# Performance work log

Measured on AMD Instinct MI355X. Metric: run time of the kernel, lower is better.

The kernel has to match this reference:

```python
import jax, jax.numpy as jnp
import numpy as np

N_NODES = 50000
N_EDGES = 800000
DIM = 128
NUM_GRAPHS = 512


def setup_inputs() -> dict:
    key = jax.random.key(0)
    ks = jax.random.split(key, 12)
    s = 1.0 / np.sqrt(DIM)
    inp = {
        'x': jax.random.normal(ks[0], (N_NODES, DIM), dtype=jnp.float32),
        'edge_index': jax.random.randint(ks[1], (2, N_EDGES), 0, N_NODES, dtype=jnp.int32),
        'batch': jnp.sort(jax.random.randint(ks[2], (N_NODES,), 0, NUM_GRAPHS, dtype=jnp.int32)),
        'W1a': jax.random.uniform(ks[3], (DIM, DIM), jnp.float32, -s, s),
        'b1a': jax.random.uniform(ks[4], (DIM,), jnp.float32, -s, s),
        'W1b': jax.random.uniform(ks[5], (DIM, DIM), jnp.float32, -s, s),
        'b1b': jax.random.uniform(ks[6], (DIM,), jnp.float32, -s, s),
        'W2a': jax.random.uniform(ks[7], (DIM, DIM), jnp.float32, -s, s),
        'b2a': jax.random.uniform(ks[8], (DIM,), jnp.float32, -s, s),
        'W2b': jax.random.uniform(ks[9], (DIM, DIM), jnp.float32, -s, s),
        'b2b': jax.random.uniform(ks[10], (DIM,), jnp.float32, -s, s),
    }
    return inp


def _gin_conv(x, edge_index, Wa, ba, Wb, bb):
    # GINConv with eps=0: h_i = MLP(x_i + sum_{j->i} x_j)
    src, dst = edge_index[0], edge_index[1]
    agg = jax.ops.segment_sum(x[src], dst, num_segments=x.shape[0])  # [N, F]
    h = x + agg
    h = jax.nn.relu(h @ Wa + ba)
    return h @ Wb + bb


def reference(x, edge_index, batch, W1a, b1a, W1b, b1b, W2a, b2a, W2b, b2b):
    h = _gin_conv(x, edge_index, W1a, b1a, W1b, b1b)
    h = _gin_conv(h, edge_index, W2a, b2a, W2b, b2b)
    # global mean pool over graphs
    sums = jax.ops.segment_sum(h, batch, num_segments=NUM_GRAPHS)      # [G, F]
    counts = jax.ops.segment_sum(jnp.ones((h.shape[0],), h.dtype), batch, num_segments=NUM_GRAPHS)
    return sums / jnp.maximum(counts, 1.0)[:, None]
```

## Files before the change

### kernel.cpp

```cpp
#include <hip/hip_runtime.h>

#define DIM 128
#define NBUCK 784
#define EPB 8192
#define ELDS_CAP 2048

typedef unsigned short ushortT;
typedef unsigned int uintT;
typedef __attribute__((ext_vector_type(8))) __bf16 bf16x8;
typedef __attribute__((ext_vector_type(4))) float f32x4;

__device__ inline ushortT f2bf(float f) {
    union { float f; uintT u; } v; v.f = f;
    uintT u = v.u;
    uintT r = (u + 0x7FFFu + ((u >> 16) & 1u)) >> 16;
    return (ushortT)r;
}
__device__ inline float bfu_lo(uintT u) { union { uintT u; float f; } v; v.u = u << 16; return v.f; }
__device__ inline float bfu_hi(uintT u) { union { uintT u; float f; } v; v.u = u & 0xffff0000u; return v.f; }
__device__ inline float bfs(ushortT s) { union { uintT u; float f; } v; v.u = ((uintT)s) << 16; return v.f; }

__device__ inline int off_in_row(int k) {
    return (((k >> 5) * 4 + ((k & 15) >> 2)) << 4) + (((k >> 4) & 1) << 3) + ((k & 3) << 1);
}

__device__ inline int wave_iscan(int v) {
    int lane = threadIdx.x & 63;
    #pragma unroll
    for (int d = 1; d < 64; d <<= 1) {
        int t = __shfl_up(v, d, 64);
        if (lane >= d) v += t;
    }
    return v;
}

__global__ __launch_bounds__(256)
void scan_carry_kernel(int* __restrict__ a, int n) {
    __shared__ int ws[4];
    __shared__ int s_carry;
    const int tid = threadIdx.x;
    const int lane = tid & 63, wv = tid >> 6;
    if (tid == 0) s_carry = 0;
    __syncthreads();
    for (int base = 0; base < n; base += 256) {
        const int i = base + tid;
        int v = (i < n) ? a[i] : 0;
        int isc = wave_iscan(v);
        if (lane == 63) ws[wv] = isc;
        __syncthreads();
        const int c = s_carry;
        if (tid == 0) { int run = 0; for (int w = 0; w < 4; ++w) { int t = ws[w]; ws[w] = run; run += t; } }
        __syncthreads();
        const int e = c + ws[wv] + isc - v;
        if (i < n) a[i] = e;
        __syncthreads();
        if (tid == 255) s_carry = e + v;
        __syncthreads();
    }
}

__global__ __launch_bounds__(256)
void scan_blk_kernel(int* __restrict__ a, int n, int* __restrict__ bsum) {
    __shared__ int ws[4];
    const int tid = threadIdx.x;
    const int i = blockIdx.x * 256 + tid;
    const int lane = tid & 63, wv = tid >> 6;
    int v = (i < n) ? a[i] : 0;
    int isc = wave_iscan(v);
    if (lane == 63) ws[wv] = isc;
    __syncthreads();
    if (tid == 0) { int run = 0; for (int w = 0; w < 4; ++w) { int t = ws[w]; ws[w] = run; run += t; } }
    __syncthreads();
    int e = ws[wv] + isc - v;
    if (i < n) a[i] = e;
    if (tid == 255) bsum[blockIdx.x] = e + v;
}

__global__ __launch_bounds__(256)
void scan_add_kernel(int* __restrict__ a, int n, const int* __restrict__ bsum) {
    int i = blockIdx.x * 256 + threadIdx.x;
    if (i < n) a[i] += bsum[blockIdx.x];
}

__global__ __launch_bounds__(256)
void histA_kernel(const int* __restrict__ dstIdx, int* __restrict__ histg, int ne, int nblk) {
    __shared__ int h[NBUCK];
    const int j = blockIdx.x;
    for (int i = threadIdx.x; i < NBUCK; i += 256) h[i] = 0;
    __syncthreads();
    const int base = j * EPB;
    const int end = (base + EPB < ne) ? base + EPB : ne;
    for (int i = base + threadIdx.x; i < end; i += 256)
        atomicAdd(&h[dstIdx[i] >> 6], 1);
    __syncthreads();
    for (int b = threadIdx.x; b < NBUCK; b += 256)
        histg[b * nblk + j] = h[b];
}

__global__ __launch_bounds__(256)
void fillA_kernel(const int* __restrict__ srcIdx, const int* __restrict__ dstIdx,
                  const int* __restrict__ Sg, uintT* __restrict__ pairs, int ne, int nblk) {
    __shared__ int cur[NBUCK];
    const int j = blockIdx.x;
    for (int i = threadIdx.x; i < NBUCK; i += 256) cur[i] = Sg[i * nblk + j];
    __syncthreads();
    const int base = j * EPB;
    const int end = (base + EPB < ne) ? base + EPB : ne;
    for (int i = base + threadIdx.x; i < end; i += 256) {
        const int d = dstIdx[i];
        const int b = d >> 6;
        const int pos = atomicAdd(&cur[b], 1);
        pairs[pos] = ((uintT)srcIdx[i] << 6) | (uintT)(d & 63);
    }
}

__global__ __launch_bounds__(256)
void convert_prep_kernel(const float* __restrict__ x, ushortT* __restrict__ xb, int n,
                         const float* __restrict__ W0, const float* __restrict__ W1,
                         const float* __restrict__ W2, const float* __restrict__ W3,
                         ushortT* __restrict__ Wt) {
    if (blockIdx.x < 128) {
        int w = blockIdx.x >> 5;
        const float* W = (w == 0) ? W0 : (w == 1) ? W1 : (w == 2) ? W2 : W3;
        ushortT* dst = Wt + (size_t)w * DIM * DIM;
        int i = (blockIdx.x & 31) * 256 + threadIdx.x;
        int nidx = i >> 6, p = i & 63, k = 2 * p;
        float w0 = W[k * DIM + nidx];
        float w1 = W[(k + 1) * DIM + nidx];
        uintT u = ((uintT)f2bf(w1) << 16) | f2bf(w0);
        *(uintT*)((char*)dst + (size_t)nidx * 256 + (off_in_row(k) ^ ((nidx & 7) << 4))) = u;
        return;
    }
    int i = (blockIdx.x - 128) * 256 + threadIdx.x;
    int node = i >> 6, p = i & 63;
    if (node >= n) return;
    float2 v = *(const float2*)(x + (size_t)node * DIM + 2 * p);
    uintT u = ((uintT)f2bf(v.y) << 16) | f2bf(v.x);
    *(uintT*)((char*)xb + (size_t)node * 256 + (off_in_row(2 * p) ^ ((node & 7) << 4))) = u;
}

__global__ __launch_bounds__(128)
void graphoff_zero_kernel(const int* __restrict__ batch, int* __restrict__ goff,
                          float* __restrict__ out, int ng, int nn) {
    const int g = blockIdx.x;
    out[(size_t)g * DIM + threadIdx.x] = 0.0f;
    if (threadIdx.x == 0) {
        int lo = 0, hi = nn;
        while (lo < hi) { int mid = (lo + hi) >> 1; if (batch[mid] < g) lo = mid + 1; else hi = mid; }
        goff[g] = lo;
    }
}

template<int POOL>
__global__ __launch_bounds__(256, 4)
void fused_kernel(const ushortT* __restrict__ Xsrc, ushortT* __restrict__ Yg,
                  const uintT* __restrict__ pairs, const int* __restrict__ Sg, int nblk,
                  const ushortT* __restrict__ WtA, const float* __restrict__ ba,
                  const ushortT* __restrict__ WtB, const float* __restrict__ bb,
                  const int* __restrict__ batch, float* __restrict__ out, int n, int ne) {
    __shared__ __align__(16) ushortT XsU[64 * DIM];
    __shared__ int elds[ELDS_CAP];
    __shared__ int histc[64];
    __shared__ int lstart[65];
    __shared__ int bs[64];

    const int b = blockIdx.x;
    const int node0 = b * 64;
    const int tid = threadIdx.x;
    const int lane = tid & 63, wid = tid >> 6;

    const int base = Sg[b * nblk];
    const int endp = (b + 1 < NBUCK) ? Sg[(b + 1) * nblk] : ne;
    int cnt = endp - base;
    if (cnt > ELDS_CAP) cnt = ELDS_CAP;

    if (tid < 64) {
        histc[tid] = 0;
        if (POOL) { int node = node0 + tid; bs[tid] = (node < n) ? batch[node] : -1; }
    }
    __syncthreads();
    for (int i = tid; i < cnt; i += 256) atomicAdd(&histc[pairs[base + i] & 63], 1);
    __syncthreads();
    if (tid < 64) {
        int v = histc[tid];
        int isc = wave_iscan(v);
        lstart[tid] = isc - v;
        histc[tid] = isc - v;
        if (tid == 63) lstart[64] = isc;
    }
    __syncthreads();
    for (int i = tid; i < cnt; i += 256) {
        uintT p = pairs[base + i];
        int pos = atomicAdd(&histc[p & 63], 1);
        elds[pos] = (int)(p >> 6);
    }
    __syncthreads();

    const int l15 = lane & 15, g16 = lane >> 4;
    const char* Xc = (const char*)Xsrc;
    for (int t = 0; t < 16; ++t) {
        const int r = wid * 16 + t;
        const int node = node0 + r;
        float acc[8];
        #pragma unroll
        for (int j = 0; j < 8; ++j) acc[j] = 0.0f;
        if (node < n) {
            if (g16 == 0) {
                uint4 v = *(const uint4*)(Xc + (size_t)node * 256 + ((l15 ^ (node & 7)) << 4));
                acc[0] += bfu_lo(v.x); acc[1] += bfu_hi(v.x);
                acc[2] += bfu_lo(v.y); acc[3] += bfu_hi(v.y);
                acc[4] += bfu_lo(v.z); acc[5] += bfu_hi(v.z);
                acc[6] += bfu_lo(v.w); acc[7] += bfu_hi(v.w);
            }
            const int s0 = lstart[r], s1 = lstart[r + 1];
            int e = s0;
            for (; e + 8 <= s1; e += 8) {
                const int sa = elds[e + g16];
                const int sb = elds[e + 4 + g16];
                uint4 va = *(const uint4*)(Xc + (size_t)sa * 256 + ((l15 ^ (sa & 7)) << 4));
                uint4 vb = *(const uint4*)(Xc + (size_t)sb * 256 + ((l15 ^ (sb & 7)) << 4));
                acc[0] += bfu_lo(va.x) + bfu_lo(vb.x); acc[1] += bfu_hi(va.x) + bfu_hi(vb.x);
                acc[2] += bfu_lo(va.y) + bfu_lo(vb.y); acc[3] += bfu_hi(va.y) + bfu_hi(vb.y);
                acc[4] += bfu_lo(va.z) + bfu_lo(vb.z); acc[5] += bfu_hi(va.z) + bfu_hi(vb.z);
                acc[6] += bfu_lo(va.w) + bfu_lo(vb.w); acc[7] += bfu_hi(va.w) + bfu_hi(vb.w);
            }
            if (e + 4 <= s1) {
                const int s = elds[e + g16];
                uint4 v = *(const uint4*)(Xc + (size_t)s * 256 + ((l15 ^ (s & 7)) << 4));
                acc[0] += bfu_lo(v.x); acc[1] += bfu_hi(v.x);
                acc[2] += bfu_lo(v.y); acc[3] += bfu_hi(v.y);
                acc[4] += bfu_lo(v.z); acc[5] += bfu_hi(v.z);
                acc[6] += bfu_lo(v.w); acc[7] += bfu_hi(v.w);
                e += 4;
            }
            const int rem = s1 - e;
            if (g16 < rem) {
                const int s = elds[e + g16];
                uint4 v = *(const uint4*)(Xc + (size_t)s * 256 + ((l15 ^ (s & 7)) << 4));
                acc[0] += bfu_lo(v.x); acc[1] += bfu_hi(v.x);
                acc[2] += bfu_lo(v.y); acc[3] += bfu_hi(v.y);
                acc[4] += bfu_lo(v.z); acc[5] += bfu_hi(v.z);
                acc[6] += bfu_lo(v.w); acc[7] += bfu_hi(v.w);
            }
        }
        #pragma unroll
        for (int j = 0; j < 8; ++j) {
            acc[j] += __shfl_xor(acc[j], 16);
            acc[j] += __shfl_xor(acc[j], 32);
        }
        if (lane < 16) {
            uint4 o;
            o.x = ((uintT)f2bf(acc[1]) << 16) | f2bf(acc[0]);
            o.y = ((uintT)f2bf(acc[3]) << 16) | f2bf(acc[2]);
            o.z = ((uintT)f2bf(acc[5]) << 16) | f2bf(acc[4]);
            o.w = ((uintT)f2bf(acc[7]) << 16) | f2bf(acc[6]);
            *(uint4*)((char*)XsU + r * 256 + ((l15 ^ (r & 7)) << 4)) = o;
        }
    }
    __syncthreads();

    const char* Xl = (const char*)XsU;
    const char* Wa = (const char*)WtA;
    const char* Wb = (const char*)WtB;
    const int g = lane >> 4;
    const int RB = (wid >> 1) * 32, CB = (wid & 1) * 64;

    f32x4 acc2[2][4];
    #pragma unroll
    for (int nt = 0; nt < 4; ++nt) {
        float bv = ba[CB + nt * 16 + l15];
        #pragma unroll
        for (int mt = 0; mt < 2; ++mt) acc2[mt][nt] = (f32x4){bv, bv, bv, bv};
    }
    #pragma unroll
    for (int ks = 0; ks < 4; ++ks) {
        const int cb = (ks * 4 + g) << 4;
        bf16x8 a0, a1, bf[4];
        { int r0 = RB + l15, r1 = RB + 16 + l15;
          a0 = *(const bf16x8*)(Xl + r0 * 256 + (cb ^ ((r0 & 7) << 4)));
          a1 = *(const bf16x8*)(Xl + r1 * 256 + (cb ^ ((r1 & 7) << 4))); }
        #pragma unroll
        for (int nt = 0; nt < 4; ++nt) {
            int rn = CB + nt * 16 + l15;
            bf[nt] = *(const bf16x8*)(Wa + rn * 256 + (cb ^ ((rn & 7) << 4)));
        }
        #pragma unroll
        for (int nt = 0; nt < 4; ++nt) {
            acc2[0][nt] = __builtin_amdgcn_mfma_f32_16x16x32_bf16(a0, bf[nt], acc2[0][nt], 0, 0, 0);
            acc2[1][nt] = __builtin_amdgcn_mfma_f32_16x16x32_bf16(a1, bf[nt], acc2[1][nt], 0, 0, 0);
        }
    }
    #pragma unroll
    for (int mt = 0; mt < 2; ++mt)
        #pragma unroll
        for (int nt = 0; nt < 4; ++nt)
            #pragma unroll
            for (int c = 0; c < 4; ++c) acc2[mt][nt][c] = fmaxf(acc2[mt][nt][c], 0.0f);

    __syncthreads();

    #pragma unroll
    for (int nt = 0; nt < 4; ++nt) {
        const int k = CB + nt * 16 + l15;
        const int offk = off_in_row(k);
        #pragma unroll
        for (int mt = 0; mt < 2; ++mt)
            #pragma unroll
            for (int r = 0; r < 4; ++r) {
                int row = RB + mt * 16 + 4 * g + r;
                *(ushortT*)((char*)XsU + row * 256 + (offk ^ ((row & 7) << 4))) = f2bf(acc2[mt][nt][r]);
            }
    }
    __syncthreads();

    #pragma unroll
    for (int nt = 0; nt < 4; ++nt) {
        float bv = bb[CB + nt * 16 + l15];
        #pragma unroll
        for (int mt = 0; mt < 2; ++mt) acc2[mt][nt] = (f32x4){bv, bv, bv, bv};
    }
    #pragma unroll
    for (int ks = 0; ks < 4; ++ks) {
        const int cb = (ks * 4 + g) << 4;
        bf16x8 a0, a1, bf[4];
        { int r0 = RB + l15, r1 = RB + 16 + l15;
          a0 = *(const bf16x8*)(Xl + r0 * 256 + (cb ^ ((r0 & 7) << 4)));
          a1 = *(const bf16x8*)(Xl + r1 * 256 + (cb ^ ((r1 & 7) << 4))); }
        #pragma unroll
        for (int nt = 0; nt < 4; ++nt) {
            int rn = CB + nt * 16 + l15;
            bf[nt] = *(const bf16x8*)(Wb + rn * 256 + (cb ^ ((rn & 7) << 4)));
        }
        #pragma unroll
        for (int nt = 0; nt < 4; ++nt) {
            acc2[0][nt] = __builtin_amdgcn_mfma_f32_16x16x32_bf16(a0, bf[nt], acc2[0][nt], 0, 0, 0);
            acc2[1][nt] = __builtin_amdgcn_mfma_f32_16x16x32_bf16(a1, bf[nt], acc2[1][nt], 0, 0, 0);
        }
    }

    if (POOL) {
        __syncthreads();
        #pragma unroll
        for (int nt = 0; nt < 4; ++nt) {
            const int k = CB + nt * 16 + l15;
            const int offk = off_in_row(k);
            #pragma unroll
            for (int mt = 0; mt < 2; ++mt)
                #pragma unroll
                for (int r = 0; r < 4; ++r) {
                    int row = RB + mt * 16 + 4 * g + r;
                    *(ushortT*)((char*)XsU + row * 256 + (offk ^ ((row & 7) << 4))) = f2bf(acc2[mt][nt][r]);
                }
        }
        __syncthreads();
        const int col = tid & 127, rh = tid >> 7;
        const int offc = off_in_row(col);
        const int r0 = rh * 32, r1 = r0 + 32;
        float run = 0.0f;
        int gcur = bs[r0];
        for (int r = r0; r < r1; ++r) {
            int gb = bs[r];
            if (gb != gcur) {
                if (gcur >= 0) atomicAdd(&out[(size_t)gcur * DIM + col], run);
                run = 0.0f; gcur = gb;
            }
            run += bfs(*(const ushortT*)((const char*)XsU + r * 256 + (offc ^ ((r & 7) << 4))));
        }
        if (gcur >= 0) atomicAdd(&out[(size_t)gcur * DIM + col], run);
    } else {
        #pragma unroll
        for (int nt = 0; nt < 4; ++nt) {
            const int k = CB + nt * 16 + l15;
            const int offk = off_in_row(k);
            #pragma unroll
            for (int mt = 0; mt < 2; ++mt)
                #pragma unroll
                for (int r = 0; r < 4; ++r) {
                    int row = RB + mt * 16 + 4 * g + r;
                    int node = node0 + row;
                    if (node < n)
                        *(ushortT*)((char*)Yg + (size_t)node * 256 + (offk ^ ((row & 7) << 4))) = f2bf(acc2[mt][nt][r]);
                }
        }
    }
}

__global__ __launch_bounds__(256)
void divide_kernel(float* __restrict__ out, const int* __restrict__ goff, int ng, int nn) {
    int i = blockIdx.x * 256 + threadIdx.x;
    if (i >= ng * DIM) return;
    int gidx = i >> 7;
    int cnt = ((gidx + 1 < ng) ? goff[gidx + 1] : nn) - goff[gidx];
    out[i] /= fmaxf((float)cnt, 1.0f);
}

extern "C" void kernel_launch(void* const* d_in, const int* in_sizes, int n_in,
                              void* d_out, int out_size, void* d_ws, size_t ws_size,
                              hipStream_t stream) {
    const float* x     = (const float*)d_in[0];
    const int*   ei    = (const int*)d_in[1];
    const int*   batch = (const int*)d_in[2];
    const float* W1a = (const float*)d_in[3];
    const float* b1a = (const float*)d_in[4];
    const float* W1b = (const float*)d_in[5];
    const float* b1b = (const float*)d_in[6];
    const float* W2a = (const float*)d_in[7];
    const float* b2a = (const float*)d_in[8];
    const float* W2b = (const float*)d_in[9];
    const float* b2b = (const float*)d_in[10];
    float* out = (float*)d_out;

    const int NN = in_sizes[0] / DIM;
    const int NE = in_sizes[1] / 2;
    const int NG = out_size / DIM;
    const int NN2 = (NN + 63) & ~63;
    const int nblk = (NE + EPB - 1) / EPB;
    const int nS = NBUCK * nblk;
    const int nScanBlk = (nS + 255) / 256;

    ushortT* xb    = (ushortT*)d_ws;
    ushortT* bufB  = xb   + (size_t)NN2 * DIM;
    ushortT* wt    = bufB + (size_t)NN2 * DIM;
    uintT*   pairs = (uintT*)(wt + 4 * DIM * DIM);
    int*     Sg    = (int*)(pairs + (size_t)NE);
    int*     bsum  = Sg + nS;
    int*     goff  = bsum + nScanBlk;

    const int* srcIdx = ei;
    const int* dstIdx = ei + NE;

    histA_kernel<<<nblk, 256, 0, stream>>>(dstIdx, Sg, NE, nblk);
    scan_blk_kernel<<<nScanBlk, 256, 0, stream>>>(Sg, nS, bsum);
    scan_carry_kernel<<<1, 256, 0, stream>>>(bsum, nScanBlk);
    scan_add_kernel<<<nScanBlk, 256, 0, stream>>>(Sg, nS, bsum);
    fillA_kernel<<<nblk, 256, 0, stream>>>(srcIdx, dstIdx, Sg, pairs, NE, nblk);

    convert_prep_kernel<<<128 + (NN * 64) / 256, 256, 0, stream>>>(x, xb, NN, W1a, W1b, W2a, W2b, wt);
    graphoff_zero_kernel<<<NG, 128, 0, stream>>>(batch, goff, out, NG, NN);

    fused_kernel<0><<<NBUCK, 256, 0, stream>>>(xb, bufB, pairs, Sg, nblk,
                                               wt, b1a, wt + DIM * DIM, b1b,
                                               batch, out, NN, NE);
    fused_kernel<1><<<NBUCK, 256, 0, stream>>>(bufB, (ushortT*)nullptr, pairs, Sg, nblk,
                                               wt + 2 * DIM * DIM, b2a, wt + 3 * DIM * DIM, b2b,
                                               batch, out, NN, NE);

    divide_kernel<<<(out_size + 255) / 256, 256, 0, stream>>>(out, goff, NG, NN);
}
```

Measured before the change: 151.9 us.

## Use 512-thread blocks in fused GIN kernel and merge scan carry into add

The fused aggregation+MLP kernel now runs 8 waves per block instead of 4. Each wave aggregates 8 rows rather than 16, and the MFMA tiles are split so each wave computes a 32x32 output block. Separately, the single-block carry scan is removed: each scan_add block sums the preceding block totals itself. This cuts one serial launch but adds redundant reads of bsum. The larger block should raise latency hiding in the gather-bound aggregation, at the cost of more barrier participants and possible occupancy limits from LDS.

```diff
diff --git a/kernel.cpp b/kernel.cpp
--- a/kernel.cpp
+++ b/kernel.cpp
@@ -32,31 +32,6 @@
         if (lane >= d) v += t;
     }
     return v;
-}
-
-__global__ __launch_bounds__(256)
-void scan_carry_kernel(int* __restrict__ a, int n) {
-    __shared__ int ws[4];
-    __shared__ int s_carry;
-    const int tid = threadIdx.x;
-    const int lane = tid & 63, wv = tid >> 6;
-    if (tid == 0) s_carry = 0;
-    __syncthreads();
-    for (int base = 0; base < n; base += 256) {
-        const int i = base + tid;
-        int v = (i < n) ? a[i] : 0;
-        int isc = wave_iscan(v);
-        if (lane == 63) ws[wv] = isc;
-        __syncthreads();
-        const int c = s_carry;
-        if (tid == 0) { int run = 0; for (int w = 0; w < 4; ++w) { int t = ws[w]; ws[w] = run; run += t; } }
-        __syncthreads();
-        const int e = c + ws[wv] + isc - v;
-        if (i < n) a[i] = e;
-        __syncthreads();
-        if (tid == 255) s_carry = e + v;
-        __syncthreads();
-    }
 }
 
 __global__ __launch_bounds__(256)
@@ -77,9 +52,20 @@
 }
 
 __global__ __launch_bounds__(256)
-void scan_add_kernel(int* __restrict__ a, int n, const int* __restrict__ bsum) {
-    int i = blockIdx.x * 256 + threadIdx.x;
-    if (i < n) a[i] += bsum[blockIdx.x];
+void scan_add2_kernel(int* __restrict__ a, int n, const int* __restrict__ bsum) {
+    __shared__ int ws[4];
+    __shared__ int s_carry;
+    const int tid = threadIdx.x;
+    int partial = 0;
+    for (int i = tid; i < (int)blockIdx.x; i += 256) partial += bsum[i];
+    #pragma unroll
+    for (int d = 1; d < 64; d <<= 1) partial += __shfl_xor(partial, d, 64);
+    if ((tid & 63) == 0) ws[tid >> 6] = partial;
+    __syncthreads();
+    if (tid == 0) s_carry = ws[0] + ws[1] + ws[2] + ws[3];
+    __syncthreads();
+    int i = blockIdx.x * 256 + tid;
+    if (i < n) a[i] += s_carry;
 }
 
 __global__ __launch_bounds__(256)
@@ -152,7 +138,7 @@
 }
 
 template<int POOL>
-__global__ __launch_bounds__(256, 4)
+__global__ __launch_bounds__(512, 4)
 void fused_kernel(const ushortT* __restrict__ Xsrc, ushortT* __restrict__ Yg,
                   const uintT* __restrict__ pairs, const int* __restrict__ Sg, int nblk,
                   const ushortT* __restrict__ WtA, const float* __restrict__ ba,
@@ -179,7 +165,7 @@
         if (POOL) { int node = node0 + tid; bs[tid] = (node < n) ? batch[node] : -1; }
     }
     __syncthreads();
-    for (int i = tid; i < cnt; i += 256) atomicAdd(&histc[pairs[base + i] & 63], 1);
+    for (int i = tid; i < cnt; i += 512) atomicAdd(&histc[pairs[base + i] & 63], 1);
     __syncthreads();
     if (tid < 64) {
         int v = histc[tid];
@@ -189,7 +175,7 @@
         if (tid == 63) lstart[64] = isc;
     }
     __syncthreads();
-    for (int i = tid; i < cnt; i += 256) {
+    for (int i = tid; i < cnt; i += 512) {
         uintT p = pairs[base + i];
         int pos = atomicAdd(&histc[p & 63], 1);
         elds[pos] = (int)(p >> 6);
@@ -198,8 +184,8 @@
 
     const int l15 = lane & 15, g16 = lane >> 4;
     const char* Xc = (const char*)Xsrc;
-    for (int t = 0; t < 16; ++t) {
-        const int r = wid * 16 + t;
+    for (int t = 0; t < 8; ++t) {
+        const int r = wid * 8 + t;
         const int node = node0 + r;
         float acc[8];
         #pragma unroll
@@ -263,11 +249,11 @@
     const char* Wa = (const char*)WtA;
     const char* Wb = (const char*)WtB;
     const int g = lane >> 4;
-    const int RB = (wid >> 1) * 32, CB = (wid & 1) * 64;
-
-    f32x4 acc2[2][4];
-    #pragma unroll
-    for (int nt = 0; nt < 4; ++nt) {
+    const int RB = (wid >> 2) * 32, CB = (wid & 3) * 32;
+
+    f32x4 acc2[2][2];
+    #pragma unroll
+    for (int nt = 0; nt < 2; ++nt) {
         float bv = ba[CB + nt * 16 + l15];
         #pragma unroll
         for (int mt = 0; mt < 2; ++mt) acc2[mt][nt] = (f32x4){bv, bv, bv, bv};
@@ -275,17 +261,17 @@
     #pragma unroll
     for (int ks = 0; ks < 4; ++ks) {
         const int cb = (ks * 4 + g) << 4;
-        bf16x8 a0, a1, bf[4];
+        bf16x8 a0, a1, bf[2];
         { int r0 = RB + l15, r1 = RB + 16 + l15;
           a0 = *(const bf16x8*)(Xl + r0 * 256 + (cb ^ ((r0 & 7) << 4)));
           a1 = *(const bf16x8*)(Xl + r1 * 256 + (cb ^ ((r1 & 7) << 4))); }
         #pragma unroll
-        for (int nt = 0; nt < 4; ++nt) {
+        for (int nt = 0; nt < 2; ++nt) {
             int rn = CB + nt * 16 + l15;
             bf[nt] = *(const bf16x8*)(Wa + rn * 256 + (cb ^ ((rn & 7) << 4)));
         }
         #pragma unroll
-        for (int nt = 0; nt < 4; ++nt) {
+        for (int nt = 0; nt < 2; ++nt) {
             acc2[0][nt] = __builtin_amdgcn_mfma_f32_16x16x32_bf16(a0, bf[nt], acc2[0][nt], 0, 0, 0);
             acc2[1][nt] = __builtin_amdgcn_mfma_f32_16x16x32_bf16(a1, bf[nt], acc2[1][nt], 0, 0, 0);
         }
@@ -293,14 +279,14 @@
     #pragma unroll
     for (int mt = 0; mt < 2; ++mt)
         #pragma unroll
-        for (int nt = 0; nt < 4; ++nt)
+        for (int nt = 0; nt < 2; ++nt)
             #pragma unroll
             for (int c = 0; c < 4; ++c) acc2[mt][nt][c] = fmaxf(acc2[mt][nt][c], 0.0f);
 
     __syncthreads();
 
     #pragma unroll
-    for (int nt = 0; nt < 4; ++nt) {
+    for (int nt = 0; nt < 2; ++nt) {
         const int k = CB + nt * 16 + l15;
         const int offk = off_in_row(k);
         #pragma unroll
@@ -314,7 +300,7 @@
     __syncthreads();
 
     #pragma unroll
-    for (int nt = 0; nt < 4; ++nt) {
+    for (int nt = 0; nt < 2; ++nt) {
         float bv = bb[CB + nt * 16 + l15];
         #pragma unroll
         for (int mt = 0; mt < 2; ++mt) acc2[mt][nt] = (f32x4){bv, bv, bv, bv};
@@ -322,17 +308,17 @@
     #pragma unroll
     for (int ks = 0; ks < 4; ++ks) {
         const int cb = (ks * 4 + g) << 4;
-        bf16x8 a0, a1, bf[4];
+        bf16x8 a0, a1, bf[2];
         { int r0 = RB + l15, r1 = RB + 16 + l15;
           a0 = *(const bf16x8*)(Xl + r0 * 256 + (cb ^ ((r0 & 7) << 4)));
           a1 = *(const bf16x8*)(Xl + r1 * 256 + (cb ^ ((r1 & 7) << 4))); }
         #pragma unroll
-        for (int nt = 0; nt < 4; ++nt) {
+        for (int nt = 0; nt < 2; ++nt) {
             int rn = CB + nt * 16 + l15;
             bf[nt] = *(const bf16x8*)(Wb + rn * 256 + (cb ^ ((rn & 7) << 4)));
         }
         #pragma unroll
-        for (int nt = 0; nt < 4; ++nt) {
+        for (int nt = 0; nt < 2; ++nt) {
             acc2[0][nt] = __builtin_amdgcn_mfma_f32_16x16x32_bf16(a0, bf[nt], acc2[0][nt], 0, 0, 0);
             acc2[1][nt] = __builtin_amdgcn_mfma_f32_16x16x32_bf16(a1, bf[nt], acc2[1][nt], 0, 0, 0);
         }
@@ -341,7 +327,7 @@
     if (POOL) {
         __syncthreads();
         #pragma unroll
-        for (int nt = 0; nt < 4; ++nt) {
+        for (int nt = 0; nt < 2; ++nt) {
             const int k = CB + nt * 16 + l15;
             const int offk = off_in_row(k);
             #pragma unroll
@@ -355,7 +341,7 @@
         __syncthreads();
         const int col = tid & 127, rh = tid >> 7;
         const int offc = off_in_row(col);
-        const int r0 = rh * 32, r1 = r0 + 32;
+        const int r0 = rh * 16, r1 = r0 + 16;
         float run = 0.0f;
         int gcur = bs[r0];
         for (int r = r0; r < r1; ++r) {
@@ -369,7 +355,7 @@
         if (gcur >= 0) atomicAdd(&out[(size_t)gcur * DIM + col], run);
     } else {
         #pragma unroll
-        for (int nt = 0; nt < 4; ++nt) {
+        for (int nt = 0; nt < 2; ++nt) {
             const int k = CB + nt * 16 + l15;
             const int offk = off_in_row(k);
             #pragma unroll
@@ -431,17 +417,16 @@
 
     histA_kernel<<<nblk, 256, 0, stream>>>(dstIdx, Sg, NE, nblk);
     scan_blk_kernel<<<nScanBlk, 256, 0, stream>>>(Sg, nS, bsum);
-    scan_carry_kernel<<<1, 256, 0, stream>>>(bsum, nScanBlk);
-    scan_add_kernel<<<nScanBlk, 256, 0, stream>>>(Sg, nS, bsum);
+    scan_add2_kernel<<<nScanBlk, 256, 0, stream>>>(Sg, nS, bsum);
     fillA_kernel<<<nblk, 256, 0, stream>>>(srcIdx, dstIdx, Sg, pairs, NE, nblk);
 
     convert_prep_kernel<<<128 + (NN * 64) / 256, 256, 0, stream>>>(x, xb, NN, W1a, W1b, W2a, W2b, wt);
     graphoff_zero_kernel<<<NG, 128, 0, stream>>>(batch, goff, out, NG, NN);
 
-    fused_kernel<0><<<NBUCK, 256, 0, stream>>>(xb, bufB, pairs, Sg, nblk,
+    fused_kernel<0><<<NBUCK, 512, 0, stream>>>(xb, bufB, pairs, Sg, nblk,
                                                wt, b1a, wt + DIM * DIM, b1b,
                                                batch, out, NN, NE);
-    fused_kernel<1><<<NBUCK, 256, 0, stream>>>(bufB, (ushortT*)nullptr, pairs, Sg, nblk,
+    fused_kernel<1><<<NBUCK, 512, 0, stream>>>(bufB, (ushortT*)nullptr, pairs, Sg, nblk,
                                                wt + 2 * DIM * DIM, b2a, wt + 3 * DIM * DIM, b2b,
                                                batch, out, NN, NE);
 
```

Result: faster. 140.8 us (-7.3%).
